# Kernel tuning notes

Hardware: AMD Instinct MI355X
Metric: run time of the kernel (lower is better)

Reference implementation:

```python
import math
import jax, jax.numpy as jnp
import numpy as np

# ---------- static Cl(3,0,0) algebra tables ----------
_BLADES = [(), (1,), (2,), (3,), (1, 2), (1, 3), (2, 3), (1, 2, 3)]
N_BLADES = 8
SUBSPACES = np.array([1, 3, 3, 1])
GRADE = np.array([len(b) for b in _BLADES])  # blade index -> grade

def _blade_mul(a, b):
    idx = list(a) + list(b)
    sign = 1
    changed = True
    while changed:
        changed = False
        for t in range(len(idx) - 1):
            if idx[t] > idx[t + 1]:
                idx[t], idx[t + 1] = idx[t + 1], idx[t]
                sign = -sign
                changed = True
    out = []
    t = 0
    while t < len(idx):
        if t + 1 < len(idx) and idx[t] == idx[t + 1]:
            t += 2  # e_i e_i = +1 (Euclidean metric)
        else:
            out.append(idx[t]); t += 1
    return sign, tuple(out)

# cayley[i, j, k]: e_i * e_k contributes sign to blade j (matches einsum 'bni,nijk,bnk->bnj')
CAYLEY = np.zeros((N_BLADES, N_BLADES, N_BLADES), dtype=np.float32)
for i, ba in enumerate(_BLADES):
    for k, bb in enumerate(_BLADES):
        s, res = _blade_mul(ba, bb)
        CAYLEY[i, _BLADES.index(res), k] = s

_starts = np.concatenate([[0], np.cumsum(SUBSPACES)[:-1]])
_paths = np.zeros((4, 4, 4), dtype=bool)
for gi in range(4):
    for gj in range(4):
        for gk in range(4):
            si, sj, sk = _starts[gi], _starts[gj], _starts[gk]
            blk = CAYLEY[si:si + SUBSPACES[gi], sj:sj + SUBSPACES[gj], sk:sk + SUBSPACES[gk]]
            _paths[gi, gj, gk] = np.any(blk != 0)
_grade_idx = np.argwhere(_paths)  # row-major order, matches torch.nonzero
N_PATHS = len(_grade_idx)  # 20 for Cl(3,0)

_bi, _bj, _bk, _pidx, _cv = [], [], [], [], []
for p, (gi, gj, gk) in enumerate(_grade_idx):
    for bi in range(_starts[gi], _starts[gi] + SUBSPACES[gi]):
        for bj in range(_starts[gj], _starts[gj] + SUBSPACES[gj]):
            for bk in range(_starts[gk], _starts[gk] + SUBSPACES[gk]):
                c = CAYLEY[bi, bj, bk]
                if c != 0:
                    _bi.append(bi); _bj.append(bj); _bk.append(bk)
                    _pidx.append(p); _cv.append(c)
BI = np.array(_bi); BJ = np.array(_bj); BK = np.array(_bk)
PIDX = np.array(_pidx); CV = np.array(_cv, dtype=np.float32)  # E = 64 nonzero entries

G_ONEHOT = (GRADE[:, None] == np.arange(4)[None, :]).astype(np.float32)  # (8, 4)

B, N_IN, N_OUT = 2048, 512, 512
EPS = 1e-6

def setup_inputs() -> dict:
    key = jax.random.key(0)
    k = jax.random.split(key, 6)
    x = jax.random.normal(k[0], (B, N_IN, N_BLADES), jnp.float32)
    weight = jax.random.normal(k[1], (N_OUT, N_IN, N_PATHS), jnp.float32) / math.sqrt(N_IN * 4)
    w_right = jax.random.normal(k[2], (N_IN, N_IN, 4), jnp.float32) / math.sqrt(N_IN)
    w_left = jax.random.normal(k[3], (N_OUT, N_IN, 4), jnp.float32) / math.sqrt(N_IN)
    b_left = jax.random.normal(k[4], (N_OUT,), jnp.float32) * 0.01
    norm_a = jnp.zeros((1, N_IN, 4), jnp.float32)  # normalization_init = 0
    return dict(x=x, weight=weight, w_right=w_right, w_left=w_left, b_left=b_left, norm_a=norm_a)

def _mvlinear(x, w):
    # w: (out, in, n_grades) -> per-blade weight via grade lookup (repeat_interleave)
    return jnp.einsum('bni,mni->bmi', x, w[:, :, GRADE])

def reference(x, weight, w_right, w_left, b_left, norm_a):
    # linear_right (no bias)
    xr = _mvlinear(x, w_right)
    # NormalizationLayer: per-grade norm, sigmoid-gated rescale toward 1
    norms = jnp.sqrt(jnp.einsum('bni,ig->bng', xr * xr, G_ONEHOT))  # (B, n, 4)
    factor = jax.nn.sigmoid(norm_a) * (norms - 1.0) + 1.0
    xr = xr / (factor[:, :, GRADE] + EPS)
    # sparse bilinear geometric product: only the 64 nonzero cayley entries
    pair = x[:, :, BI] * xr[:, :, BK]            # (B, n, E)
    wsel = weight[:, :, PIDX] * CV               # (m, n, E)
    tmp = jnp.einsum('bne,mne->bme', pair, wsel)  # (B, m, E)
    bilinear = jnp.zeros((x.shape[0], weight.shape[0], N_BLADES), x.dtype).at[:, :, BJ].add(tmp)
    # linear_left with bias embedded on the scalar blade (index 0)
    left = _mvlinear(x, w_left).at[:, :, 0].add(b_left)
    return (left + bilinear) / math.sqrt(2.0)
```

## Files before the change

### kernel.cpp

```cpp
#include <hip/hip_runtime.h>
#include <stdint.h>


#define B_DIM 2048
#define N_DIM 512
#define PLANE (B_DIM * N_DIM)
#define WPLANE (N_DIM * N_DIM)
#define KTOT (9 * N_DIM)

using frag8 = __attribute__((ext_vector_type(8))) short;
using f32x4 = __attribute__((ext_vector_type(4))) float;

__device__ __forceinline__ float bf2f(unsigned short u) {
  union { unsigned int i; float f; } v;
  v.i = ((unsigned int)u) << 16;
  return v.f;
}
__device__ __forceinline__ unsigned short f2bf(float f) {
  unsigned int u = __float_as_uint(f);
  return (unsigned short)((u + 0x7FFFu + ((u >> 16) & 1u)) >> 16);
}
__device__ __forceinline__ unsigned int pairpack(unsigned int a, unsigned int r) {
  const float pe = __uint_as_float(a << 16) * __uint_as_float(r << 16);
  const float po = __uint_as_float(a & 0xFFFF0000u) * __uint_as_float(r & 0xFFFF0000u);
  return __builtin_amdgcn_perm(__float_as_uint(po) + 0x8000u,
                               __float_as_uint(pe) + 0x8000u, 0x07060302u);
}

typedef const unsigned int __attribute__((address_space(1)))* gas_t;
typedef unsigned int __attribute__((address_space(3)))* las_t;
__device__ __forceinline__ void gload16(const void* g, void* l) {
  __builtin_amdgcn_global_load_lds((gas_t)g, (las_t)l, 16, 0, 0);
}

#define SGN_INIT {                                                     \
  {0,0,0,0,0x8000,0x8000,0x8000,0x8000},                               \
  {0,0,0,0,0x8000,0x8000,0x8000,0x8000},                               \
  {0,0x8000,0,0,0,0,0x8000,0},                                         \
  {0,0x8000,0x8000,0,0x8000,0,0,0x8000},                               \
  {0,0x8000,0,0,0,0,0x8000,0},                                         \
  {0,0x8000,0x8000,0,0x8000,0,0,0x8000},                               \
  {0,0,0x8000,0,0,0x8000,0,0},                                         \
  {0,0,0x8000,0,0,0x8000,0,0} }
#define PJK_INIT {                                                     \
  {0,4,4,4,10,10,10,16},  {5,1,11,11,6,6,17,12},                       \
  {5,11,1,11,6,17,6,12},  {5,11,11,1,17,6,6,12},                       \
  {13,7,7,18,2,14,14,8},  {13,7,18,7,14,2,14,8},                       \
  {13,18,7,7,14,14,2,8},  {19,15,15,15,9,9,9,3} }
#define GR_INIT {0,1,1,1,2,2,2,3}


__global__ __launch_bounds__(256) void repack_x(const float* __restrict__ x,
                                                unsigned short* __restrict__ xt) {
  const int t = blockIdx.x * 256 + threadIdx.x;
  const float4 v0 = *(const float4*)(x + (size_t)t * 8);
  const float4 v1 = *(const float4*)(x + (size_t)t * 8 + 4);
  const float v[8] = {v0.x, v0.y, v0.z, v0.w, v1.x, v1.y, v1.z, v1.w};
#pragma unroll
  for (int i = 0; i < 8; ++i) xt[(size_t)i * PLANE + t] = f2bf(v[i]);
}

__global__ __launch_bounds__(256) void repack_wr(const float* __restrict__ wr,
                                                 unsigned short* __restrict__ wrt) {
  const int t = blockIdx.x * 256 + threadIdx.x;
  const float4 v = *(const float4*)(wr + (size_t)t * 4);
  const float p[4] = {v.x, v.y, v.z, v.w};
#pragma unroll
  for (int g = 0; g < 4; ++g) wrt[(size_t)g * WPLANE + t] = f2bf(p[g]);
}

__global__ __launch_bounds__(256) void build_W(const float* __restrict__ w,
                                               const float* __restrict__ wl,
                                               unsigned short* __restrict__ Wall) {
  constexpr int PJK[8][8] = PJK_INIT;
  constexpr unsigned short SGN[8][8] = SGN_INIT;
  constexpr int GR[8] = GR_INIT;
  const int t = blockIdx.x * 256 + threadIdx.x;
  const int m = t >> 9, n = t & 511;
  const float* wrow = w + (size_t)t * 20;
  const float* wlrow = wl + (size_t)t * 4;
  unsigned short w20[20];
#pragma unroll
  for (int p = 0; p < 20; ++p) w20[p] = f2bf(wrow[p]);
  unsigned short wl4[4];
#pragma unroll
  for (int g = 0; g < 4; ++g) wl4[g] = f2bf(wlrow[g]);
#pragma unroll
  for (int j = 0; j < 8; ++j) {
    const size_t base = ((size_t)j * N_DIM + m) * KTOT + n;
#pragma unroll
    for (int k = 0; k < 8; ++k)
      Wall[base + (size_t)k * N_DIM] = (unsigned short)(w20[PJK[j][k]] ^ SGN[j][k]);
    Wall[base + (size_t)8 * N_DIM] = wl4[GR[j]];
  }
}

__global__ __launch_bounds__(256) void normk(unsigned short* __restrict__ xre,
                                             const float* __restrict__ na) {
  const int t = blockIdx.x * 256 + threadIdx.x;
  const int n = t & 511;
  float v[8];
#pragma unroll
  for (int p = 0; p < 8; ++p) v[p] = bf2f(xre[(size_t)p * PLANE + t]);
  const float n0 = fabsf(v[0]);
  const float n1 = sqrtf(v[1] * v[1] + v[2] * v[2] + v[3] * v[3]);
  const float n2 = sqrtf(v[4] * v[4] + v[5] * v[5] + v[6] * v[6]);
  const float n3 = fabsf(v[7]);
  float f[4];
  const float nm[4] = {n0, n1, n2, n3};
#pragma unroll
  for (int g = 0; g < 4; ++g) {
    const float a = na[n * 4 + g];
    const float sig = 1.0f / (1.0f + __expf(-a));
    f[g] = sig * (nm[g] - 1.0f) + 1.0f + 1e-6f;
  }
  v[0] /= f[0];
  v[1] /= f[1]; v[2] /= f[1]; v[3] /= f[1];
  v[4] /= f[2]; v[5] /= f[2]; v[6] /= f[2];
  v[7] /= f[3];
#pragma unroll
  for (int p = 0; p < 8; ++p) xre[(size_t)p * PLANE + t] = f2bf(v[p]);
  xre[(size_t)8 * PLANE + t] = 0x3F80;
}


__global__ __launch_bounds__(256, 3) void gemm1(const unsigned short* __restrict__ xt,
                                                const unsigned short* __restrict__ wrt,
                                                unsigned short* __restrict__ xre) {
  constexpr int GR[8] = GR_INIT;
  __shared__ __attribute__((aligned(16))) unsigned short sA[2][4096];
  __shared__ __attribute__((aligned(16))) unsigned short sB[2][4096];
  const int bm0 = blockIdx.x * 128, bn0 = blockIdx.y * 128, z = blockIdx.z;
  const unsigned short* A = xt + (size_t)z * PLANE;
  const unsigned short* Bm = wrt + (size_t)GR[z] * WPLANE;
  unsigned short* C = xre + (size_t)z * PLANE;

  const int tid = (int)threadIdx.x;
  const int l = tid & 63, w = tid >> 6;
  const int wm = (w >> 1) * 64, wn = (w & 1) * 64;
  const int fr = l & 15, quad = l >> 4, msw = (fr >> 1) & 3;
  const int rdA = (wm + fr) * 32 + (quad ^ msw) * 8;
  const int rdB = (wn + fr) * 32 + (quad ^ msw) * 8;
  const int ks = (((l & 3) ^ ((l >> 3) & 3))) * 8;
  const int r0 = w * 32 + (l >> 2);
  const unsigned short* pa0 = A + (size_t)(bm0 + r0) * N_DIM + ks;
  const unsigned short* pa1 = pa0 + (size_t)16 * N_DIM;
  const unsigned short* pb0 = Bm + (size_t)(bn0 + r0) * N_DIM + ks;
  const unsigned short* pb1 = pb0 + (size_t)16 * N_DIM;
  const int db = w * 1024;

  f32x4 acc[4][4];
#pragma unroll
  for (int mt = 0; mt < 4; ++mt)
#pragma unroll
    for (int nt = 0; nt < 4; ++nt) acc[mt][nt] = (f32x4){0.f, 0.f, 0.f, 0.f};

  gload16(pa0, &sA[0][db]);
  gload16(pa1, &sA[0][db + 512]);
  gload16(pb0, &sB[0][db]);
  gload16(pb1, &sB[0][db + 512]);
  __syncthreads();

#pragma unroll 2
  for (int it = 0; it < 16; ++it) {
    const int cur = it & 1;
    if (it < 15) {
      const int off = (it + 1) * 32;
      gload16(pa0 + off, &sA[cur ^ 1][db]);
      gload16(pa1 + off, &sA[cur ^ 1][db + 512]);
      gload16(pb0 + off, &sB[cur ^ 1][db]);
      gload16(pb1 + off, &sB[cur ^ 1][db + 512]);
    }
    frag8 af[4], bf[4];
#pragma unroll
    for (int t = 0; t < 4; ++t) af[t] = *(const frag8*)&sA[cur][rdA + t * 512];
#pragma unroll
    for (int t = 0; t < 4; ++t) bf[t] = *(const frag8*)&sB[cur][rdB + t * 512];
#pragma unroll
    for (int mt = 0; mt < 4; ++mt)
#pragma unroll
      for (int nt = 0; nt < 4; ++nt)
        acc[mt][nt] = __builtin_amdgcn_mfma_f32_16x16x32_bf16(af[mt], bf[nt], acc[mt][nt], 0, 0, 0);
    __syncthreads();
  }
#pragma unroll
  for (int mt = 0; mt < 4; ++mt) {
    const int row0 = bm0 + wm + mt * 16 + quad * 4;
#pragma unroll
    for (int nt = 0; nt < 4; ++nt) {
      const int col = bn0 + wn + nt * 16 + fr;
#pragma unroll
      for (int r = 0; r < 4; ++r)
        C[(size_t)(row0 + r) * N_DIM + col] = f2bf(acc[mt][nt][r]);
    }
  }
}


__global__ __launch_bounds__(256, 3) void gemm2(const unsigned short* __restrict__ xt,
                                                const unsigned short* __restrict__ xre,
                                                const unsigned short* __restrict__ Wall,
                                                const float* __restrict__ bl,
                                                float* __restrict__ out) {
  __shared__ __attribute__((aligned(16))) unsigned short sA[2][4096];
  __shared__ __attribute__((aligned(16))) unsigned short sB[2][4096];
  const int bm0 = blockIdx.x * 128, bn0 = blockIdx.y * 128, j = blockIdx.z;

  const int tid = (int)threadIdx.x;
  const int l = tid & 63, w = tid >> 6;
  const int wm = (w >> 1) * 64, wn = (w & 1) * 64;
  const int fr = l & 15, quad = l >> 4, msw = (fr >> 1) & 3;
  const int rdA = (wm + fr) * 32 + (quad ^ msw) * 8;
  const int rdB = (wn + fr) * 32 + (quad ^ msw) * 8;
  const int ks = (((l & 3) ^ ((l >> 3) & 3))) * 8;
  const int r0 = w * 32 + (l >> 2);
  const int db = w * 1024;
  const int pj = (j == 3 || j == 4) ? (j ^ 7) : j;

  const size_t ar0 = (size_t)(bm0 + r0) * N_DIM + (l & 3) * 8;
  const size_t ar1 = ar0 + (size_t)16 * N_DIM;
  const int wr0 = r0 * 32 + ks, wr1 = wr0 + 512;
  const unsigned short* pw0 = Wall + ((size_t)j * N_DIM + bn0 + r0) * KTOT + ks;
  const unsigned short* pw1 = pw0 + (size_t)16 * KTOT;

  auto ieof = [&](int sl) -> int {
    int ps = (sl == 3 || sl == 4) ? (sl ^ 7) : sl;
    int ix = pj ^ ps;
    ix = (ix == 3 || ix == 4) ? (ix ^ 7) : ix;
    return (sl == 8) ? j : ix;
  };

  f32x4 acc[4][4];
#pragma unroll
  for (int mt = 0; mt < 4; ++mt)
#pragma unroll
    for (int nt = 0; nt < 4; ++nt) acc[mt][nt] = (f32x4){0.f, 0.f, 0.f, 0.f};

  {
    const unsigned short* bx = xt + ((size_t)ieof(0)) * PLANE;
    const uint4 x0 = *(const uint4*)(bx + ar0);
    const uint4 e0 = *(const uint4*)(xre + ar0);
    const uint4 x1 = *(const uint4*)(bx + ar1);
    const uint4 e1 = *(const uint4*)(xre + ar1);
    gload16(pw0, &sB[0][db]);
    gload16(pw1, &sB[0][db + 512]);
    uint4 o0, o1;
    o0.x = pairpack(x0.x, e0.x); o0.y = pairpack(x0.y, e0.y);
    o0.z = pairpack(x0.z, e0.z); o0.w = pairpack(x0.w, e0.w);
    o1.x = pairpack(x1.x, e1.x); o1.y = pairpack(x1.y, e1.y);
    o1.z = pairpack(x1.z, e1.z); o1.w = pairpack(x1.w, e1.w);
    *(uint4*)&sA[0][wr0] = o0;
    *(uint4*)&sA[0][wr1] = o1;
  }
  __syncthreads();

#pragma unroll 2
  for (int it = 0; it < 144; ++it) {
    const int cur = it & 1;
    uint4 x0, e0, x1, e1;
    if (it < 143) {
      const int kn = it + 1;
      const int sl = kn >> 4, n0 = (kn & 15) << 5;
      int ps = (sl == 3 || sl == 4) ? (sl ^ 7) : sl;
      int ix = pj ^ ps;
      ix = (ix == 3 || ix == 4) ? (ix ^ 7) : ix;
      const int ie = (sl == 8) ? j : ix;
      const unsigned short* bx = xt + (size_t)ie * PLANE;
      const unsigned short* be = xre + (size_t)sl * PLANE;
      x0 = *(const uint4*)(bx + ar0 + n0);
      e0 = *(const uint4*)(be + ar0 + n0);
      x1 = *(const uint4*)(bx + ar1 + n0);
      e1 = *(const uint4*)(be + ar1 + n0);
      gload16(pw0 + (size_t)kn * 32, &sB[cur ^ 1][db]);
      gload16(pw1 + (size_t)kn * 32, &sB[cur ^ 1][db + 512]);
    }
    frag8 af[4], bf[4];
#pragma unroll
    for (int t = 0; t < 4; ++t) af[t] = *(const frag8*)&sA[cur][rdA + t * 512];
#pragma unroll
    for (int t = 0; t < 4; ++t) bf[t] = *(const frag8*)&sB[cur][rdB + t * 512];
#pragma unroll
    for (int mt = 0; mt < 4; ++mt)
#pragma unroll
      for (int nt = 0; nt < 4; ++nt)
        acc[mt][nt] = __builtin_amdgcn_mfma_f32_16x16x32_bf16(af[mt], bf[nt], acc[mt][nt], 0, 0, 0);
    if (it < 143) {
      uint4 o0, o1;
      o0.x = pairpack(x0.x, e0.x); o0.y = pairpack(x0.y, e0.y);
      o0.z = pairpack(x0.z, e0.z); o0.w = pairpack(x0.w, e0.w);
      o1.x = pairpack(x1.x, e1.x); o1.y = pairpack(x1.y, e1.y);
      o1.z = pairpack(x1.z, e1.z); o1.w = pairpack(x1.w, e1.w);
      *(uint4*)&sA[cur ^ 1][wr0] = o0;
      *(uint4*)&sA[cur ^ 1][wr1] = o1;
    }
    __syncthreads();
  }

  const float inv = 0.70710678118654752f;
#pragma unroll
  for (int nt = 0; nt < 4; ++nt) {
    const int col = bn0 + wn + nt * 16 + fr;
    const float bias = (j == 0) ? bl[col] : 0.0f;
#pragma unroll
    for (int mt = 0; mt < 4; ++mt) {
      const int row0 = bm0 + wm + mt * 16 + quad * 4;
#pragma unroll
      for (int r = 0; r < 4; ++r)
        out[((size_t)(row0 + r) * N_DIM + col) * 8 + j] =
            (acc[mt][nt][r] + bias) * inv;
    }
  }
}


extern "C" void kernel_launch(void* const* d_in, const int* in_sizes, int n_in,
                              void* d_out, int out_size, void* d_ws, size_t ws_size,
                              hipStream_t stream) {
  const float* x = (const float*)d_in[0];
  const float* w = (const float*)d_in[1];
  const float* wr = (const float*)d_in[2];
  const float* wl = (const float*)d_in[3];
  const float* bl = (const float*)d_in[4];
  const float* na = (const float*)d_in[5];
  float* out = (float*)d_out;

  char* ws = (char*)d_ws;
  unsigned short* xt = (unsigned short*)(ws);
  unsigned short* xre = (unsigned short*)(ws + 16777216);
  unsigned short* wrt = (unsigned short*)(ws + 35651584);
  unsigned short* Wall = (unsigned short*)(ws + 37748736);

  repack_x<<<4096, 256, 0, stream>>>(x, xt);
  repack_wr<<<1024, 256, 0, stream>>>(wr, wrt);
  build_W<<<1024, 256, 0, stream>>>(w, wl, Wall);
  gemm1<<<dim3(16, 4, 8), 256, 0, stream>>>(xt, wrt, xre);
  normk<<<4096, 256, 0, stream>>>(xre, na);
  gemm2<<<dim3(16, 4, 8), 256, 0, stream>>>(xt, xre, Wall, bl, out);
}
```

Baseline: 307.8 us.

## Split gemm2 K dimension in two with separate partial buffer and reduction kernel

Splits the 144-step K loop of gemm2 into two 72-step segments, doubling the grid so more blocks fill the GPU. The second segment writes to a workspace buffer and a new elementwise kernel adds it into the output. Launch bounds are raised to target four blocks per CU. This costs an extra full-size fp32 write, read and rewrite of the output plus another kernel launch.

```diff
diff --git a/kernel.cpp b/kernel.cpp
--- a/kernel.cpp
+++ b/kernel.cpp
@@ -197,14 +197,19 @@
 }
 
 
-__global__ __launch_bounds__(256, 3) void gemm2(const unsigned short* __restrict__ xt,
+__global__ __launch_bounds__(256, 4) void gemm2(const unsigned short* __restrict__ xt,
                                                 const unsigned short* __restrict__ xre,
                                                 const unsigned short* __restrict__ Wall,
                                                 const float* __restrict__ bl,
-                                                float* __restrict__ out) {
+                                                float* __restrict__ out,
+                                                float* __restrict__ pp) {
   __shared__ __attribute__((aligned(16))) unsigned short sA[2][4096];
   __shared__ __attribute__((aligned(16))) unsigned short sB[2][4096];
-  const int bm0 = blockIdx.x * 128, bn0 = blockIdx.y * 128, j = blockIdx.z;
+  const int bm0 = blockIdx.x * 128;
+  const int bn0 = ((int)blockIdx.y & 3) * 128;
+  const int seg = (int)blockIdx.y >> 2;
+  const int j = blockIdx.z;
+  const int kc0 = seg * 72;
 
   const int tid = (int)threadIdx.x;
   const int l = tid & 63, w = tid >> 6;
@@ -237,13 +242,15 @@
     for (int nt = 0; nt < 4; ++nt) acc[mt][nt] = (f32x4){0.f, 0.f, 0.f, 0.f};
 
   {
-    const unsigned short* bx = xt + ((size_t)ieof(0)) * PLANE;
-    const uint4 x0 = *(const uint4*)(bx + ar0);
-    const uint4 e0 = *(const uint4*)(xre + ar0);
-    const uint4 x1 = *(const uint4*)(bx + ar1);
-    const uint4 e1 = *(const uint4*)(xre + ar1);
-    gload16(pw0, &sB[0][db]);
-    gload16(pw1, &sB[0][db + 512]);
+    const int sl0 = kc0 >> 4, n00 = (kc0 & 15) << 5;
+    const unsigned short* bx = xt + (size_t)ieof(sl0) * PLANE;
+    const unsigned short* be = xre + (size_t)sl0 * PLANE;
+    const uint4 x0 = *(const uint4*)(bx + ar0 + n00);
+    const uint4 e0 = *(const uint4*)(be + ar0 + n00);
+    const uint4 x1 = *(const uint4*)(bx + ar1 + n00);
+    const uint4 e1 = *(const uint4*)(be + ar1 + n00);
+    gload16(pw0 + (size_t)kc0 * 32, &sB[0][db]);
+    gload16(pw1 + (size_t)kc0 * 32, &sB[0][db + 512]);
     uint4 o0, o1;
     o0.x = pairpack(x0.x, e0.x); o0.y = pairpack(x0.y, e0.y);
     o0.z = pairpack(x0.z, e0.z); o0.w = pairpack(x0.w, e0.w);
@@ -255,11 +262,11 @@
   __syncthreads();
 
 #pragma unroll 2
-  for (int it = 0; it < 144; ++it) {
+  for (int it = 0; it < 72; ++it) {
     const int cur = it & 1;
     uint4 x0, e0, x1, e1;
-    if (it < 143) {
-      const int kn = it + 1;
+    if (it < 71) {
+      const int kn = kc0 + it + 1;
       const int sl = kn >> 4, n0 = (kn & 15) << 5;
       int ps = (sl == 3 || sl == 4) ? (sl ^ 7) : sl;
       int ix = pj ^ ps;
@@ -284,7 +291,7 @@
 #pragma unroll
       for (int nt = 0; nt < 4; ++nt)
         acc[mt][nt] = __builtin_amdgcn_mfma_f32_16x16x32_bf16(af[mt], bf[nt], acc[mt][nt], 0, 0, 0);
-    if (it < 143) {
+    if (it < 71) {
       uint4 o0, o1;
       o0.x = pairpack(x0.x, e0.x); o0.y = pairpack(x0.y, e0.y);
       o0.z = pairpack(x0.z, e0.z); o0.w = pairpack(x0.w, e0.w);
@@ -297,19 +304,30 @@
   }
 
   const float inv = 0.70710678118654752f;
+  float* dst = (seg == 0) ? out : pp;
 #pragma unroll
   for (int nt = 0; nt < 4; ++nt) {
     const int col = bn0 + wn + nt * 16 + fr;
-    const float bias = (j == 0) ? bl[col] : 0.0f;
+    const float bias = (seg == 0 && j == 0) ? bl[col] : 0.0f;
 #pragma unroll
     for (int mt = 0; mt < 4; ++mt) {
       const int row0 = bm0 + wm + mt * 16 + quad * 4;
 #pragma unroll
       for (int r = 0; r < 4; ++r)
-        out[((size_t)(row0 + r) * N_DIM + col) * 8 + j] =
+        dst[((size_t)(row0 + r) * N_DIM + col) * 8 + j] =
             (acc[mt][nt][r] + bias) * inv;
     }
   }
+}
+
+
+__global__ __launch_bounds__(256) void addred(float* __restrict__ out,
+                                              const float* __restrict__ pp) {
+  const size_t t = ((size_t)blockIdx.x * 256 + threadIdx.x) * 4;
+  float4 a = *(float4*)(out + t);
+  const float4 b = *(const float4*)(pp + t);
+  a.x += b.x; a.y += b.y; a.z += b.z; a.w += b.w;
+  *(float4*)(out + t) = a;
 }
 
 
@@ -329,11 +347,13 @@
   unsigned short* xre = (unsigned short*)(ws + 16777216);
   unsigned short* wrt = (unsigned short*)(ws + 35651584);
   unsigned short* Wall = (unsigned short*)(ws + 37748736);
+  float* pp = (float*)(ws + 75497472);
 
   repack_x<<<4096, 256, 0, stream>>>(x, xt);
   repack_wr<<<1024, 256, 0, stream>>>(wr, wrt);
   build_W<<<1024, 256, 0, stream>>>(w, wl, Wall);
   gemm1<<<dim3(16, 4, 8), 256, 0, stream>>>(xt, wrt, xre);
   normk<<<4096, 256, 0, stream>>>(xre, na);
-  gemm2<<<dim3(16, 4, 8), 256, 0, stream>>>(xt, xre, Wall, bl, out);
-}
+  gemm2<<<dim3(16, 8, 8), 256, 0, stream>>>(xt, xre, Wall, bl, out, pp);
+  addred<<<8192, 256, 0, stream>>>(out, pp);
+}
```

Result: slower. 371.7 us (+20.8%).
